# Kernel optimization log

Hardware: AMD Instinct MI355X
Metric: run time of the kernel (lower is better)

The kernel has to match this reference:

```python
import jax, jax.numpy as jnp
import numpy as np


def setup_inputs() -> dict:
    key = jax.random.key(0)
    k1, k2, k3 = jax.random.split(key, 3)
    B, T, N = 2, 16, 128
    INP, COND, OUT = 64, 64, 128
    x = jax.random.normal(k1, (B, T, N, INP), dtype=jnp.float32)
    cond = jax.random.normal(k2, (B, N, N, COND), dtype=jnp.float32)
    in_dim = 6 * INP + 2 * COND  # 512
    W = jax.random.normal(k3, (in_dim, OUT), dtype=jnp.float32) / np.sqrt(in_dim)
    b = jnp.zeros((OUT,), dtype=jnp.float32)
    return {"x": x, "cond": cond, "W": W, "b": b}


def reference(x, cond, W, b):
    # x: (B,T,N,C), cond: (B,N,N,Cc), W: (6C+2Cc, O), b: (O,)
    B, T, N, C = x.shape
    Cc = cond.shape[-1]
    # temporal boundary-zeroed copies (faithful to torch cat of zeros + slices)
    x1 = x.at[:, 0].set(0.0)        # zeros at t=0
    x2 = x.at[:, -1].set(0.0)       # zeros at t=T-1
    xc = jnp.concatenate([x1, x, x2], axis=-1)  # (B,T,N,3C)
    # decompose the big linear over the concat [x1_pair, x2_pair, cond1, cond2]
    W1 = W[: 3 * C]
    W2 = W[3 * C: 6 * C]
    Wc1 = W[6 * C: 6 * C + Cc]
    Wc2 = W[6 * C + Cc:]
    a = jnp.einsum('btnc,co->btno', xc, W1)               # n1 contribution
    bpart = jnp.einsum('btnc,co->btno', xc, W2)            # n2 contribution
    # cond1[b,t,i,j] = cond[b,i,j]; cond2[b,t,i,j] = cond[b,j,i]
    cpart = (jnp.einsum('bijc,co->bijo', cond, Wc1)
             + jnp.einsum('bjic,co->bijo', cond, Wc2))     # (B,N,N,O)
    s = (a[:, :, :, None, :] + bpart[:, :, None, :, :]
         + cpart[:, None, :, :, :] + b)                    # (B,T,N,N,O)
    act = s * jax.nn.sigmoid(s)                            # swish
    return jnp.max(act, axis=3)                            # amax over n2 -> (B,T,N,O)
```

## Files before the change

### kernel.cpp

```cpp
#include <hip/hip_runtime.h>
#include <math.h>

#define B_ 2
#define T_ 16
#define N_ 128
#define CI 64
#define CO 128

#define AQ_OFF 0
#define BQ_OFF 524288
#define CQ_OFF 1048576

__device__ __forceinline__ float4 f4add(float4 a, float4 b) {
  return make_float4(a.x + b.x, a.y + b.y, a.z + b.z, a.w + b.w);
}
__device__ __forceinline__ float4 f4max(float4 a, float4 b) {
  return make_float4(fmaxf(a.x, b.x), fmaxf(a.y, b.y), fmaxf(a.z, b.z), fmaxf(a.w, b.w));
}
__device__ __forceinline__ float4 f4min(float4 a, float4 b) {
  return make_float4(fminf(a.x, b.x), fminf(a.y, b.y), fminf(a.z, b.z), fminf(a.w, b.w));
}
__device__ __forceinline__ void f4fma(float4& acc, float s, float4 v) {
  acc.x = fmaf(s, v.x, acc.x);
  acc.y = fmaf(s, v.y, acc.y);
  acc.z = fmaf(s, v.z, acc.z);
  acc.w = fmaf(s, v.w, acc.w);
}
__device__ __forceinline__ float silu1(float v) { return v / (1.0f + __expf(-v)); }
__device__ __forceinline__ float4 silu4(float4 v) {
  return make_float4(silu1(v.x), silu1(v.y), silu1(v.z), silu1(v.w));
}
__device__ __forceinline__ float4 shfl4x(float4 v, int m) {
  return make_float4(__shfl_xor(v.x, m, 64), __shfl_xor(v.y, m, 64),
                     __shfl_xor(v.z, m, 64), __shfl_xor(v.w, m, 64));
}

__global__ __launch_bounds__(256) void k_ab2(
    const float* __restrict__ x, const float* __restrict__ W,
    const float* __restrict__ bias, float* __restrict__ AQ, float* __restrict__ BQ)
{
  __shared__ __align__(16) float WL[64 * 128];
  __shared__ float xT[64 * 17];

  int blk = blockIdx.x;
  int nq  = blk & 7;
  int dst = (blk >> 3) & 1;
  int t   = (blk >> 4) & 15;
  int b   = blk >> 8;
  float f0 = (t != 0)      ? 1.0f : 0.0f;
  float f2 = (t != T_ - 1) ? 1.0f : 0.0f;
  int tid = threadIdx.x;

  const float4* W4 = (const float4*)W;
  float4* WL4 = (float4*)WL;
  int wb = dst * 6144;
  #pragma unroll
  for (int k = 0; k < 8; k++) {
    int idx4 = tid + k * 256;
    float4 wa = W4[wb + idx4];
    float4 wm = W4[wb + 2048 + idx4];
    float4 wc = W4[wb + 4096 + idx4];
    WL4[idx4] = make_float4(f0 * wa.x + wm.x + f2 * wc.x,
                            f0 * wa.y + wm.y + f2 * wc.y,
                            f0 * wa.z + wm.z + f2 * wc.z,
                            f0 * wa.w + wm.w + f2 * wc.w);
  }
  {
    long xb = ((long)(b * T_ + t) * N_ + nq * 16) * CI;
    #pragma unroll
    for (int k = 0; k < 4; k++) {
      int idx = tid + k * 256;
      int c = idx & 63, n = idx >> 6;
      xT[c * 17 + n] = x[xb + n * CI + c];
    }
  }
  __syncthreads();

  int nl = tid & 15;
  int qg = tid >> 4;
  float4 acc0, acc1;
  if (dst == 0) {
    acc0 = ((const float4*)bias)[qg * 2];
    acc1 = ((const float4*)bias)[qg * 2 + 1];
  } else {
    acc0 = make_float4(0, 0, 0, 0); acc1 = acc0;
  }
  #pragma unroll 8
  for (int c = 0; c < 64; c++) {
    float xv = xT[c * 17 + nl];
    float4 w0 = WL4[c * 32 + qg * 2];
    float4 w1 = WL4[c * 32 + qg * 2 + 1];
    f4fma(acc0, xv, w0);
    f4fma(acc1, xv, w1);
  }
  float* dp = dst ? BQ : AQ;
  int n = nq * 16 + nl;
  long u0 = ((long)(b * 32 + qg * 2) * 16 + t) * 128 + n;
  long u1 = u0 + 16 * 128;
  ((float4*)dp)[u0] = acc0;
  ((float4*)dp)[u1] = acc1;
}

__global__ __launch_bounds__(128) void k_cp2(
    const float* __restrict__ cond, const float* __restrict__ W,
    float* __restrict__ CQ)
{
  __shared__ __align__(16) float WL[64 * 64];
  __shared__ float Cd[64 * 65];

  int blk = blockIdx.x;
  int of = blk & 1;
  int jh = (blk >> 1) & 1;
  int i  = (blk >> 2) & 127;
  int b  = blk >> 9;
  int tid = threadIdx.x;
  int og = tid & 15;
  int jg = tid >> 4;

  float4 acc[8];
  #pragma unroll
  for (int k = 0; k < 8; k++) acc[k] = make_float4(0, 0, 0, 0);

  const float4* W4 = (const float4*)W;
  const float4* c4p = (const float4*)cond;
  float4* WL4 = (float4*)WL;

  for (int p = 0; p < 2; p++) {
    #pragma unroll
    for (int k = 0; k < 8; k++) {
      int idx4 = tid + k * 128;
      int c = idx4 >> 4, u = idx4 & 15;
      WL4[idx4] = W4[(384 + p * 64 + c) * 32 + of * 16 + u];
    }
    #pragma unroll
    for (int k = 0; k < 8; k++) {
      int idx4 = tid + k * 128;
      int jl = idx4 >> 4, c4 = idx4 & 15;
      long src = (p == 0)
        ? ((long)(b * N_ + i) * N_ + jh * 64 + jl) * 16 + c4
        : ((long)(b * N_ + jh * 64 + jl) * N_ + i) * 16 + c4;
      float4 v = c4p[src];
      float* row = &Cd[jl * 65 + c4 * 4];
      row[0] = v.x; row[1] = v.y; row[2] = v.z; row[3] = v.w;
    }
    __syncthreads();
    for (int c = 0; c < 64; c++) {
      float4 w = WL4[c * 16 + og];
      #pragma unroll
      for (int k = 0; k < 8; k++) {
        float cd = Cd[(jg * 8 + k) * 65 + c];
        f4fma(acc[k], cd, w);
      }
    }
    __syncthreads();
  }
  int oq = of * 16 + og;
  long base = ((long)(b * 32 + oq) * 128 + i) * 128 + jh * 64 + jg * 8;
  float4* CQ4 = (float4*)CQ;
  #pragma unroll
  for (int k = 0; k < 8; k++) CQ4[base + k] = acc[k];
}

__global__ __launch_bounds__(512) void k_red2(
    const float* __restrict__ AQ, const float* __restrict__ BQ,
    const float* __restrict__ CQ, float* __restrict__ out)
{
  __shared__ __align__(16) float BpL[2064 * 4];
  __shared__ __align__(16) float CpL[8 * 132 * 4];

  int blk = blockIdx.x;
  int ic = blk & 7;
  int oq = (blk >> 3) & 31;
  int b  = blk >> 8;
  int tid = threadIdx.x;

  const float4* BQ4 = (const float4*)BQ;
  const float4* CQ4 = (const float4*)CQ;
  const float4* AQ4 = (const float4*)AQ;
  float4* BpL4 = (float4*)BpL;
  float4* CpL4 = (float4*)CpL;

  long slab = (long)(b * 32 + oq) * 2048;
  #pragma unroll
  for (int k = 0; k < 4; k++) {
    int idx = tid + k * 512;
    int t = idx >> 7, j = idx & 127;
    BpL4[t * 129 + j] = BQ4[slab + idx];
  }
  __syncthreads();

  int w    = tid >> 6;
  int lane = tid & 63;
  int t    = lane >> 2;
  int js   = lane & 3;
  int cbase = w * 132;

  for (int r = 0; r < 2; r++) {
    int i = ic * 16 + w * 2 + r;
    long crow = ((long)(b * 32 + oq) * 128 + i) * 128;
    {
      int u0 = lane, u1 = lane + 64;
      CpL4[cbase + (u0 >> 5) * 33 + (u0 & 31)] = CQ4[crow + u0];
      CpL4[cbase + (u1 >> 5) * 33 + (u1 & 31)] = CQ4[crow + u1];
    }
    __syncthreads();

    float4 mxa = make_float4(-3.4e38f, -3.4e38f, -3.4e38f, -3.4e38f);
    float4 mxb = mxa;
    float4 mna = make_float4(3.4e38f, 3.4e38f, 3.4e38f, 3.4e38f);
    float4 mnb = mna;
    int bb = t * 129 + js * 32;
    int cb = cbase + js * 33;
    #pragma unroll 4
    for (int jj = 0; jj < 32; jj += 2) {
      float4 s0 = f4add(BpL4[bb + jj],     CpL4[cb + jj]);
      float4 s1 = f4add(BpL4[bb + jj + 1], CpL4[cb + jj + 1]);
      mxa = f4max(mxa, s0); mna = f4min(mna, s0);
      mxb = f4max(mxb, s1); mnb = f4min(mnb, s1);
    }
    float4 mx = f4max(mxa, mxb);
    float4 mn = f4min(mna, mnb);
    mx = f4max(mx, shfl4x(mx, 1)); mn = f4min(mn, shfl4x(mn, 1));
    mx = f4max(mx, shfl4x(mx, 2)); mn = f4min(mn, shfl4x(mn, 2));

    if (js == 0) {
      float4 av = AQ4[slab + t * 128 + i];
      float4 M  = f4add(mx, av);
      float4 Mn = f4add(mn, av);
      float4 res = f4max(silu4(M), silu4(Mn));
      ((float4*)out)[(long)((b * 16 + t) * 128 + i) * 32 + oq] = res;
    }
    __syncthreads();
  }
}

extern "C" void kernel_launch(void* const* d_in, const int* in_sizes, int n_in,
                              void* d_out, int out_size, void* d_ws, size_t ws_size,
                              hipStream_t stream) {
  const float* x    = (const float*)d_in[0];
  const float* cond = (const float*)d_in[1];
  const float* W    = (const float*)d_in[2];
  const float* bias = (const float*)d_in[3];
  float* out = (float*)d_out;

  float* ws = (float*)d_ws;
  float* AQ = ws + AQ_OFF;
  float* BQ = ws + BQ_OFF;
  float* CQ = ws + CQ_OFF;

  k_ab2<<<512, 256, 0, stream>>>(x, W, bias, AQ, BQ);
  k_cp2<<<1024, 128, 0, stream>>>(cond, W, CQ);
  k_red2<<<512, 512, 0, stream>>>(AQ, BQ, CQ, out);
}
```

Measured before the change: 110.2 us.

## Precombine boundary weights in a prep kernel and restructure max-reduction to reuse CQ in registers

Adds a small prep kernel that precomputes the three boundary-class combined weight matrices once, so the AB projection kernel copies one pre-summed tile instead of reading and combining three weight slices per block. The reduction kernel is rewritten so each thread holds a CQ row chunk in registers and reuses it across 8 timesteps, with BQ transposed into shared memory and AQ staged in LDS. This removes the per-row CQ staging and inner barriers. It adds an extra launch and a workspace buffer and raises register pressure from the 16 float4 accumulators.

```diff
diff --git a/kernel.cpp b/kernel.cpp
--- a/kernel.cpp
+++ b/kernel.cpp
@@ -10,6 +10,7 @@
 #define AQ_OFF 0
 #define BQ_OFF 524288
 #define CQ_OFF 1048576
+#define WT_OFF 5242880
 
 __device__ __forceinline__ float4 f4add(float4 a, float4 b) {
   return make_float4(a.x + b.x, a.y + b.y, a.z + b.z, a.w + b.w);
@@ -35,8 +36,31 @@
                      __shfl_xor(v.z, m, 64), __shfl_xor(v.w, m, 64));
 }
 
-__global__ __launch_bounds__(256) void k_ab2(
-    const float* __restrict__ x, const float* __restrict__ W,
+__global__ __launch_bounds__(256) void k_prep(const float* __restrict__ W,
+                                              float* __restrict__ WT) {
+  int e4 = blockIdx.x * 256 + threadIdx.x;
+  int flat = e4 * 4;
+  int cls = flat / 16384;
+  int rem = flat - cls * 16384;
+  int c = rem >> 8;
+  int oo = rem & 255;
+  float f0 = (cls == 0) ? 0.0f : 1.0f;
+  float f2 = (cls == 2) ? 0.0f : 1.0f;
+  const float4* W4 = (const float4*)W;
+  int o = oo & 127;
+  int base = (oo < 128) ? 0 : 24576;
+  int wi = (base + c * 128 + o) >> 2;
+  float4 wa = W4[wi];
+  float4 wm = W4[wi + 2048];
+  float4 wc = W4[wi + 4096];
+  ((float4*)WT)[e4] = make_float4(f0 * wa.x + wm.x + f2 * wc.x,
+                                  f0 * wa.y + wm.y + f2 * wc.y,
+                                  f0 * wa.z + wm.z + f2 * wc.z,
+                                  f0 * wa.w + wm.w + f2 * wc.w);
+}
+
+__global__ __launch_bounds__(256) void k_ab3(
+    const float* __restrict__ x, const float* __restrict__ WT,
     const float* __restrict__ bias, float* __restrict__ AQ, float* __restrict__ BQ)
 {
   __shared__ __align__(16) float WL[64 * 128];
@@ -47,23 +71,15 @@
   int dst = (blk >> 3) & 1;
   int t   = (blk >> 4) & 15;
   int b   = blk >> 8;
-  float f0 = (t != 0)      ? 1.0f : 0.0f;
-  float f2 = (t != T_ - 1) ? 1.0f : 0.0f;
+  int cls = (t == 0) ? 0 : ((t == T_ - 1) ? 2 : 1);
   int tid = threadIdx.x;
 
-  const float4* W4 = (const float4*)W;
+  const float4* WT4 = (const float4*)WT;
   float4* WL4 = (float4*)WL;
-  int wb = dst * 6144;
   #pragma unroll
   for (int k = 0; k < 8; k++) {
     int idx4 = tid + k * 256;
-    float4 wa = W4[wb + idx4];
-    float4 wm = W4[wb + 2048 + idx4];
-    float4 wc = W4[wb + 4096 + idx4];
-    WL4[idx4] = make_float4(f0 * wa.x + wm.x + f2 * wc.x,
-                            f0 * wa.y + wm.y + f2 * wc.y,
-                            f0 * wa.z + wm.z + f2 * wc.z,
-                            f0 * wa.w + wm.w + f2 * wc.w);
+    WL4[idx4] = WT4[cls * 4096 + (idx4 >> 5) * 64 + dst * 32 + (idx4 & 31)];
   }
   {
     long xb = ((long)(b * T_ + t) * N_ + nq * 16) * CI;
@@ -161,76 +177,91 @@
   for (int k = 0; k < 8; k++) CQ4[base + k] = acc[k];
 }
 
-__global__ __launch_bounds__(512) void k_red2(
+__global__ __launch_bounds__(256) void k_red4(
     const float* __restrict__ AQ, const float* __restrict__ BQ,
     const float* __restrict__ CQ, float* __restrict__ out)
 {
-  __shared__ __align__(16) float BpL[2064 * 4];
-  __shared__ __align__(16) float CpL[8 * 132 * 4];
+  __shared__ __align__(16) float4 BpL4[128 * 9];
+  __shared__ __align__(16) float4 AQL4[256];
 
   int blk = blockIdx.x;
-  int ic = blk & 7;
+  int iq = blk & 3;
+  int th = (blk >> 2) & 1;
   int oq = (blk >> 3) & 31;
   int b  = blk >> 8;
   int tid = threadIdx.x;
 
   const float4* BQ4 = (const float4*)BQ;
+  const float4* AQ4 = (const float4*)AQ;
   const float4* CQ4 = (const float4*)CQ;
-  const float4* AQ4 = (const float4*)AQ;
-  float4* BpL4 = (float4*)BpL;
-  float4* CpL4 = (float4*)CpL;
-
-  long slab = (long)(b * 32 + oq) * 2048;
+
+  long slab4 = ((long)(b * 32 + oq) * 16 + th * 8) * 128;
+
   #pragma unroll
   for (int k = 0; k < 4; k++) {
-    int idx = tid + k * 512;
+    int idx = tid + k * 256;
     int t = idx >> 7, j = idx & 127;
-    BpL4[t * 129 + j] = BQ4[slab + idx];
+    BpL4[j * 9 + t] = BQ4[slab4 + idx];
+  }
+  {
+    int t = tid >> 5, il = tid & 31;
+    AQL4[tid] = AQ4[slab4 + t * 128 + iq * 32 + il];
   }
   __syncthreads();
 
-  int w    = tid >> 6;
-  int lane = tid & 63;
-  int t    = lane >> 2;
-  int js   = lane & 3;
-  int cbase = w * 132;
-
-  for (int r = 0; r < 2; r++) {
-    int i = ic * 16 + w * 2 + r;
-    long crow = ((long)(b * 32 + oq) * 128 + i) * 128;
-    {
-      int u0 = lane, u1 = lane + 64;
-      CpL4[cbase + (u0 >> 5) * 33 + (u0 & 31)] = CQ4[crow + u0];
-      CpL4[cbase + (u1 >> 5) * 33 + (u1 & 31)] = CQ4[crow + u1];
-    }
-    __syncthreads();
-
-    float4 mxa = make_float4(-3.4e38f, -3.4e38f, -3.4e38f, -3.4e38f);
-    float4 mxb = mxa;
-    float4 mna = make_float4(3.4e38f, 3.4e38f, 3.4e38f, 3.4e38f);
-    float4 mnb = mna;
-    int bb = t * 129 + js * 32;
-    int cb = cbase + js * 33;
-    #pragma unroll 4
-    for (int jj = 0; jj < 32; jj += 2) {
-      float4 s0 = f4add(BpL4[bb + jj],     CpL4[cb + jj]);
-      float4 s1 = f4add(BpL4[bb + jj + 1], CpL4[cb + jj + 1]);
-      mxa = f4max(mxa, s0); mna = f4min(mna, s0);
-      mxb = f4max(mxb, s1); mnb = f4min(mnb, s1);
-    }
-    float4 mx = f4max(mxa, mxb);
-    float4 mn = f4min(mna, mnb);
-    mx = f4max(mx, shfl4x(mx, 1)); mn = f4min(mn, shfl4x(mn, 1));
-    mx = f4max(mx, shfl4x(mx, 2)); mn = f4min(mn, shfl4x(mn, 2));
-
-    if (js == 0) {
-      float4 av = AQ4[slab + t * 128 + i];
-      float4 M  = f4add(mx, av);
-      float4 Mn = f4add(mn, av);
+  int il = tid >> 3;
+  int je = tid & 7;
+
+  float4 mx[8], mn[8];
+  #pragma unroll
+  for (int t = 0; t < 8; t++) {
+    mx[t] = make_float4(-3.4e38f, -3.4e38f, -3.4e38f, -3.4e38f);
+    mn[t] = make_float4(3.4e38f, 3.4e38f, 3.4e38f, 3.4e38f);
+  }
+
+  const float4* CQr = CQ4 + ((long)(b * 32 + oq) * 128 + iq * 32 + il) * 128 + je;
+
+  #pragma unroll
+  for (int jj = 0; jj < 16; jj += 4) {
+    float4 c0 = CQr[(jj + 0) * 8];
+    float4 c1 = CQr[(jj + 1) * 8];
+    float4 c2 = CQr[(jj + 2) * 8];
+    float4 c3 = CQr[(jj + 3) * 8];
+    int jb0 = (je + 8 * (jj + 0)) * 9;
+    int jb1 = (je + 8 * (jj + 1)) * 9;
+    int jb2 = (je + 8 * (jj + 2)) * 9;
+    int jb3 = (je + 8 * (jj + 3)) * 9;
+    #pragma unroll
+    for (int t = 0; t < 8; t++) {
+      float4 s0 = f4add(c0, BpL4[jb0 + t]);
+      float4 s1 = f4add(c1, BpL4[jb1 + t]);
+      float4 s2 = f4add(c2, BpL4[jb2 + t]);
+      float4 s3 = f4add(c3, BpL4[jb3 + t]);
+      mx[t] = f4max(mx[t], f4max(f4max(s0, s1), f4max(s2, s3)));
+      mn[t] = f4min(mn[t], f4min(f4min(s0, s1), f4min(s2, s3)));
+    }
+  }
+
+  #pragma unroll
+  for (int t = 0; t < 8; t++) {
+    mx[t] = f4max(mx[t], shfl4x(mx[t], 1));
+    mn[t] = f4min(mn[t], shfl4x(mn[t], 1));
+    mx[t] = f4max(mx[t], shfl4x(mx[t], 2));
+    mn[t] = f4min(mn[t], shfl4x(mn[t], 2));
+    mx[t] = f4max(mx[t], shfl4x(mx[t], 4));
+    mn[t] = f4min(mn[t], shfl4x(mn[t], 4));
+  }
+
+  if (je == 0) {
+    int i = iq * 32 + il;
+    #pragma unroll
+    for (int t = 0; t < 8; t++) {
+      float4 av = AQL4[t * 32 + il];
+      float4 M  = f4add(mx[t], av);
+      float4 Mn = f4add(mn[t], av);
       float4 res = f4max(silu4(M), silu4(Mn));
-      ((float4*)out)[(long)((b * 16 + t) * 128 + i) * 32 + oq] = res;
-    }
-    __syncthreads();
+      ((float4*)out)[(long)((b * 16 + th * 8 + t) * 128 + i) * 32 + oq] = res;
+    }
   }
 }
 
@@ -247,8 +278,10 @@
   float* AQ = ws + AQ_OFF;
   float* BQ = ws + BQ_OFF;
   float* CQ = ws + CQ_OFF;
-
-  k_ab2<<<512, 256, 0, stream>>>(x, W, bias, AQ, BQ);
+  float* WT = ws + WT_OFF;
+
+  k_prep<<<48, 256, 0, stream>>>(W, WT);
+  k_ab3<<<512, 256, 0, stream>>>(x, WT, bias, AQ, BQ);
   k_cp2<<<1024, 128, 0, stream>>>(cond, W, CQ);
-  k_red2<<<512, 512, 0, stream>>>(AQ, BQ, CQ, out);
-}
+  k_red4<<<512, 256, 0, stream>>>(AQ, BQ, CQ, out);
+}
```

Result: slower. 118.3 us (+7.3%).
